# Performance work log

Measured on AMD Instinct MI355X. Metric: run time of the kernel, lower is better.

## Reference

```python
import jax, jax.numpy as jnp
import numpy as np

D_MODEL = 1024
NUM_HEADS = 16
D_K = D_MODEL // NUM_HEADS
B, T = 4, 2048


def setup_inputs() -> dict:
    key = jax.random.key(0)
    ks = jax.random.split(key, 10)
    s = 1.0 / np.sqrt(D_MODEL)
    return {
        "x": jax.random.normal(ks[0], (B, T, D_MODEL), dtype=jnp.float32),
        "attn_mask": jax.random.randint(ks[1], (B, T), 0, 2, dtype=jnp.int32),
        "wq": jax.random.uniform(ks[2], (D_MODEL, D_MODEL), jnp.float32, -s, s),
        "bq": jax.random.uniform(ks[3], (D_MODEL,), jnp.float32, -s, s),
        "wk": jax.random.uniform(ks[4], (D_MODEL, D_MODEL), jnp.float32, -s, s),
        "bk": jax.random.uniform(ks[5], (D_MODEL,), jnp.float32, -s, s),
        "wv": jax.random.uniform(ks[6], (D_MODEL, D_MODEL), jnp.float32, -s, s),
        "bv": jax.random.uniform(ks[7], (D_MODEL,), jnp.float32, -s, s),
        "wo": jax.random.uniform(ks[8], (D_MODEL, D_MODEL), jnp.float32, -s, s),
        "bo": jax.random.uniform(ks[9], (D_MODEL,), jnp.float32, -s, s),
    }


def reference(x, attn_mask, wq, bq, wk, bk, wv, bv, wo, bo):
    b, t, d = x.shape
    h, dk = NUM_HEADS, D_K
    # project and split heads: [B, H, T, Dk]
    q = (x @ wq + bq).reshape(b, t, h, dk).transpose(0, 2, 1, 3)
    k = (x @ wk + bk).reshape(b, t, h, dk).transpose(0, 2, 1, 3)
    v = (x @ wv + bv).reshape(b, t, h, dk).transpose(0, 2, 1, 3)
    scores = jnp.einsum("bhqd,bhkd->bhqk", q, k) / jnp.sqrt(jnp.float32(dk))
    mask = attn_mask[:, None, None, :]  # [B,1,1,T]
    scores = jnp.where(mask == 0, jnp.float32(-1e9), scores)
    attn = jax.nn.softmax(scores, axis=-1)
    out = jnp.einsum("bhqk,bhkd->bhqd", attn, v)
    out = out.transpose(0, 2, 1, 3).reshape(b, t, d)
    return out @ wo + bo
```

## Files before the change

kernel.cpp:

```cpp
#include <hip/hip_runtime.h>
#include <math.h>

#define TT 2048
#define DD 1024
#define HH 16
#define DKK 64
#define BB 4
#define NN 8192

typedef __bf16 bf16x8 __attribute__((ext_vector_type(8)));
typedef float f32x4 __attribute__((ext_vector_type(4)));
typedef float f32x16 __attribute__((ext_vector_type(16)));
typedef unsigned int uint2v __attribute__((ext_vector_type(2)));

#define QSCALE 0.18033688011112043f

__device__ __forceinline__ unsigned short f2bf(float f) {
  unsigned int u = __builtin_bit_cast(unsigned int, f);
  u += 0x7fffu + ((u >> 16) & 1u);
  return (unsigned short)(u >> 16);
}

__device__ __forceinline__ unsigned int cvtpk(float lo, float hi) {
  unsigned int r;
  asm("v_cvt_pk_bf16_f32 %0, %1, %2" : "=v"(r) : "v"(lo), "v"(hi));
  return r;
}

__device__ __forceinline__ void gl_lds16(const void* g, void* s) {
  __builtin_amdgcn_global_load_lds(
      (const __attribute__((address_space(1))) void*)g,
      (__attribute__((address_space(3))) void*)s, 16, 0, 0);
}

#define SWZ(r, byte) ((byte) ^ (((r) & 7) << 4))

__global__ __launch_bounds__(256) void cast_f32_bf16(
    const float* __restrict__ in, unsigned short* __restrict__ out, int n4) {
  int i = blockIdx.x * blockDim.x + threadIdx.x;
  if (i < n4) {
    float4 v = reinterpret_cast<const float4*>(in)[i];
    ushort4 o;
    o.x = f2bf(v.x); o.y = f2bf(v.y); o.z = f2bf(v.z); o.w = f2bf(v.w);
    reinterpret_cast<ushort4*>(out)[i] = o;
  }
}

__global__ __launch_bounds__(256) void wtrans(
    const float* __restrict__ W0, const float* __restrict__ W1,
    const float* __restrict__ W2, const float* __restrict__ W3,
    unsigned short* __restrict__ WT) {
  __shared__ float t[32][33];
  const float* W = (blockIdx.z == 0) ? W0
                   : (blockIdx.z == 1) ? W1
                   : (blockIdx.z == 2) ? W2 : W3;
  unsigned short* O = WT + (size_t)blockIdx.z * DD * DD;
  const int tx = threadIdx.x & 31, ty = threadIdx.x >> 5;
  const int r0 = blockIdx.y * 32, c0 = blockIdx.x * 32;
#pragma unroll
  for (int j = 0; j < 4; ++j)
    t[ty + 8 * j][tx] = W[(size_t)(r0 + ty + 8 * j) * DD + c0 + tx];
  __syncthreads();
#pragma unroll
  for (int j = 0; j < 4; ++j)
    O[(size_t)(c0 + ty + 8 * j) * DD + r0 + tx] = f2bf(t[tx][ty + 8 * j]);
}

__global__ __launch_bounds__(256) void mask_scan(
    const int* __restrict__ mask, int* __restrict__ cm, int* __restrict__ cnt) {
  __shared__ int part[256];
  const int b = blockIdx.x;
  const int tid = threadIdx.x;
  const int* mp = mask + b * TT;
  int loc[8], s = 0;
#pragma unroll
  for (int j = 0; j < 8; ++j) {
    loc[j] = mp[tid * 8 + j] ? 1 : 0;
    s += loc[j];
  }
  part[tid] = s;
  __syncthreads();
  for (int off = 1; off < 256; off <<= 1) {
    const int u = (tid >= off) ? part[tid - off] : 0;
    __syncthreads();
    part[tid] += u;
    __syncthreads();
  }
  if (tid == 255) cnt[b] = part[255];
  int run = part[tid] - s;
#pragma unroll
  for (int j = 0; j < 8; ++j) {
    cm[b * TT + tid * 8 + j] = loc[j] ? (run + 1) : 0;
    run += loc[j];
  }
}

template <int EPI>
__global__ __launch_bounds__(256) void gemm_m97(
    const unsigned short* __restrict__ A, const unsigned short* __restrict__ Bw,
    const float* __restrict__ b0, const float* __restrict__ b1,
    const float* __restrict__ b2, const int* __restrict__ cm,
    unsigned short* __restrict__ O0, unsigned short* __restrict__ O1,
    unsigned short* __restrict__ O2, float* __restrict__ Of) {
  __shared__ unsigned short As[128 * 32];
  __shared__ unsigned short Bs[128 * 32];
  const int tid = threadIdx.x;
  const int l = tid & 63, w = tid >> 6;
  const int ln = l & 15, kg = l >> 4;
  const int wr = w >> 1, wc = w & 1;
  const int rb = blockIdx.x * 128, cb = blockIdx.y * 128;

  f32x4 acc[4][4];
#pragma unroll
  for (int i = 0; i < 4; ++i)
#pragma unroll
    for (int j = 0; j < 4; ++j)
#pragma unroll
      for (int r = 0; r < 4; ++r) acc[i][j][r] = 0.f;

  const int srow = w * 16 + (l >> 2);
  const int sch = (l & 3) * 16;
  const char* Ag = (const char*)A + (size_t)(rb + srow) * 2048 + sch;
  const char* Bg = (const char*)Bw + (size_t)(cb + srow) * 2048 + sch;
  char* Ad = (char*)As + w * 1024;
  char* Bd = (char*)Bs + w * 1024;

  for (int k0 = 0; k0 < 2048; k0 += 64) {
    __syncthreads();
    gl_lds16(Ag + k0, Ad);
    gl_lds16(Ag + k0 + (size_t)64 * 2048, Ad + 4096);
    gl_lds16(Bg + k0, Bd);
    gl_lds16(Bg + k0 + (size_t)64 * 2048, Bd + 4096);
    __syncthreads();
    bf16x8 af[4], bfv[4];
#pragma unroll
    for (int mi = 0; mi < 4; ++mi)
      af[mi] = *reinterpret_cast<const bf16x8*>(
          (const char*)As + (wr * 64 + mi * 16 + ln) * 64 + kg * 16);
#pragma unroll
    for (int ni = 0; ni < 4; ++ni)
      bfv[ni] = *reinterpret_cast<const bf16x8*>(
          (const char*)Bs + (wc * 64 + ni * 16 + ln) * 64 + kg * 16);
#pragma unroll
    for (int mi = 0; mi < 4; ++mi)
#pragma unroll
      for (int ni = 0; ni < 4; ++ni)
        acc[mi][ni] = __builtin_amdgcn_mfma_f32_16x16x32_bf16(
            af[mi], bfv[ni], acc[mi][ni], 0, 0, 0);
  }

  if constexpr (EPI == 0) {
    const int sel = blockIdx.y >> 3;
    const float* bias = sel == 0 ? b0 : (sel == 1 ? b1 : b2);
    const float scale = sel == 0 ? QSCALE : 1.0f;
#pragma unroll
    for (int ni = 0; ni < 4; ++ni) {
      const int c3 = cb + wc * 64 + ni * 16 + ln;
      const int c = c3 & 1023, h = (c3 >> 6) & 15, dk = c3 & 63;
      const float bsv = bias[c];
#pragma unroll
      for (int mi = 0; mi < 4; ++mi) {
#pragma unroll
        for (int r = 0; r < 4; ++r) {
          const int rl = rb + wr * 64 + mi * 16 + kg * 4 + r;
          const int b_ = rl >> 11, t = rl & 2047, bh = b_ * HH + h;
          const unsigned short v = f2bf((acc[mi][ni][r] + bsv) * scale);
          if (sel == 0) {
            O0[(size_t)(bh * 16 + (t >> 7)) * 8192 + (dk >> 3) * 1024 +
               (t & 127) * 8 + (dk & 7)] = v;
          } else {
            const int cmv = cm[b_ * TT + t];
            if (cmv > 0) {
              const int ct = cmv - 1;
              if (sel == 1) {
                O1[(size_t)(bh * 32 + (ct >> 6)) * 4096 + (dk >> 3) * 512 +
                   ((ct >> 5) & 1) * 256 + (ct & 31) * 8 + (dk & 7)] = v;
              } else {
                O2[(size_t)(bh * 32 + (ct >> 6)) * 4096 + ((ct >> 3) & 7) * 512 +
                   (dk >> 5) * 256 + (dk & 31) * 8 + (ct & 7)] = v;
              }
            }
          }
        }
      }
    }
  } else {
#pragma unroll
    for (int ni = 0; ni < 4; ++ni) {
      const int cl = cb + wc * 64 + ni * 16 + ln;
      const float bsv = b0[cl];
#pragma unroll
      for (int mi = 0; mi < 4; ++mi)
#pragma unroll
        for (int r = 0; r < 4; ++r) {
          const int rl = rb + wr * 64 + mi * 16 + kg * 4 + r;
          Of[(size_t)rl * DD + cl] = acc[mi][ni][r] + bsv;
        }
    }
  }
}

template <bool TAIL>
__device__ __forceinline__ void attn_tile10(
    int kt, int n, const char* __restrict__ KU, const char* __restrict__ VU,
    int foff, int hi, const bf16x8 (&qf)[4], f32x16& oc0, f32x16& oc1,
    float& l_) {
  const int ktoff = kt << 13;

  f32x16 sc0, sc1;
#pragma unroll
  for (int i = 0; i < 16; ++i) { sc0[i] = 0.f; sc1[i] = 0.f; }
  __builtin_amdgcn_s_setprio(1);
#pragma unroll
  for (int s = 0; s < 4; ++s) {
    const bf16x8 kf0 =
        *reinterpret_cast<const bf16x8*>(KU + ktoff + foff + s * 2048);
    const bf16x8 kf1 =
        *reinterpret_cast<const bf16x8*>(KU + ktoff + foff + s * 2048 + 512);
    sc0 = __builtin_amdgcn_mfma_f32_32x32x16_bf16(kf0, qf[s], sc0, 0, 0, 0);
    sc1 = __builtin_amdgcn_mfma_f32_32x32x16_bf16(kf1, qf[s], sc1, 0, 0, 0);
  }
  __builtin_amdgcn_s_setprio(0);

  bf16x8 vf[8];
#pragma unroll
  for (int s = 0; s < 4; ++s) {
    vf[2 * s] = *reinterpret_cast<const bf16x8*>(VU + ktoff + foff + s * 2048);
    vf[2 * s + 1] =
        *reinterpret_cast<const bf16x8*>(VU + ktoff + foff + s * 2048 + 512);
  }

#pragma unroll
  for (int i = 0; i < 16; ++i) sc0[i] = __builtin_exp2f(sc0[i]);
#pragma unroll
  for (int i = 0; i < 16; ++i) sc1[i] = __builtin_exp2f(sc1[i]);

  if (TAIL) {
    const int kvb = (kt << 6) + 4 * hi;
#pragma unroll
    for (int i = 0; i < 16; ++i) {
      const int kv0 = kvb + (i & 3) + 8 * (i >> 2);
      sc0[i] = (kv0 < n) ? sc0[i] : 0.f;
      sc1[i] = (kv0 + 32 < n) ? sc1[i] : 0.f;
    }
  }

  {
    const float ra = ((sc0[0] + sc0[1]) + (sc0[2] + sc0[3])) +
                     ((sc0[4] + sc0[5]) + (sc0[6] + sc0[7]));
    const float rb2 = ((sc0[8] + sc0[9]) + (sc0[10] + sc0[11])) +
                      ((sc0[12] + sc0[13]) + (sc0[14] + sc0[15]));
    const float rc = ((sc1[0] + sc1[1]) + (sc1[2] + sc1[3])) +
                     ((sc1[4] + sc1[5]) + (sc1[6] + sc1[7]));
    const float rd = ((sc1[8] + sc1[9]) + (sc1[10] + sc1[11])) +
                     ((sc1[12] + sc1[13]) + (sc1[14] + sc1[15]));
    l_ += (ra + rb2) + (rc + rd);
  }

  bf16x8 pf[4];
#pragma unroll
  for (int s = 0; s < 4; ++s) {
    const int u = s & 1;
    float p0, p1, p2, p3, p4, p5, p6, p7;
    if ((s >> 1) == 0) {
      p0 = sc0[8 * u + 0]; p1 = sc0[8 * u + 1]; p2 = sc0[8 * u + 2];
      p3 = sc0[8 * u + 3]; p4 = sc0[8 * u + 4]; p5 = sc0[8 * u + 5];
      p6 = sc0[8 * u + 6]; p7 = sc0[8 * u + 7];
    } else {
      p0 = sc1[8 * u + 0]; p1 = sc1[8 * u + 1]; p2 = sc1[8 * u + 2];
      p3 = sc1[8 * u + 3]; p4 = sc1[8 * u + 4]; p5 = sc1[8 * u + 5];
      p6 = sc1[8 * u + 6]; p7 = sc1[8 * u + 7];
    }
    const unsigned int wa0 = cvtpk(p0, p1), wa1 = cvtpk(p2, p3);
    const unsigned int wb0 = cvtpk(p4, p5), wb1 = cvtpk(p6, p7);
    const uint2v r0 = __builtin_amdgcn_permlane32_swap(wa0, wb0, false, false);
    const uint2v r1 = __builtin_amdgcn_permlane32_swap(wa1, wb1, false, false);
    union { unsigned int u4[4]; bf16x8 v; } pw;
    pw.u4[0] = r0.x;
    pw.u4[1] = r1.x;
    pw.u4[2] = r0.y;
    pw.u4[3] = r1.y;
    pf[s] = pw.v;
  }

  __builtin_amdgcn_s_setprio(1);
#pragma unroll
  for (int s = 0; s < 4; ++s) {
    oc0 = __builtin_amdgcn_mfma_f32_32x32x16_bf16(vf[2 * s], pf[s], oc0, 0, 0, 0);
    oc1 = __builtin_amdgcn_mfma_f32_32x32x16_bf16(vf[2 * s + 1], pf[s], oc1, 0, 0, 0);
  }
  __builtin_amdgcn_s_setprio(0);
}

__global__ __launch_bounds__(256) void attn_v10(
    const unsigned short* __restrict__ Qt, const unsigned short* __restrict__ Kt,
    const unsigned short* __restrict__ Vt, const int* __restrict__ cnt,
    unsigned short* __restrict__ Ab) {
  const int id = blockIdx.x + 16 * blockIdx.y;
  const int bh = id & 63, qt = id >> 6;
  const int b = bh >> 4, h = bh & 15;

  __shared__ __align__(16) char lds[16384];

  const int tid = threadIdx.x;
  const int l = tid & 63, w = tid >> 6;
  const int ln = l & 31, hi = l >> 5;

  const char* Qtile = (const char*)Qt + (size_t)(bh * 16 + qt) * 16384;
  const char* KU = (const char*)Kt + ((size_t)bh << 18);
  const char* VU = (const char*)Vt + ((size_t)bh << 18);
  const int n = cnt[b];
  const int ntile = (n + 63) >> 6;

  const int qrow = w * 32 + ln;
  bf16x8 qf[4];
#pragma unroll
  for (int s = 0; s < 4; ++s)
    qf[s] = *reinterpret_cast<const bf16x8*>(
        Qtile + (size_t)(s * 2 + hi) * 2048 + qrow * 16);

  const int foff = hi * 1024 + ln * 16;

  f32x16 oc0, oc1;
#pragma unroll
  for (int i = 0; i < 16; ++i) { oc0[i] = 0.f; oc1[i] = 0.f; }
  float l_ = 0.f;

  for (int kt = 0; kt + 1 < ntile; ++kt)
    attn_tile10<false>(kt, n, KU, VU, foff, hi, qf, oc0, oc1, l_);
  attn_tile10<true>(ntile - 1, n, KU, VU, foff, hi, qf, oc0, oc1, l_);

  float ls = l_ + __shfl_xor(l_, 32);
  const float inv = 1.0f / ls;
#pragma unroll
  for (int i = 0; i < 16; ++i) { oc0[i] *= inv; oc1[i] *= inv; }
#pragma unroll
  for (int g = 0; g < 4; ++g) {
    const int d0a = 8 * g + 4 * hi;
    uint2 wv;
    wv.x = cvtpk(oc0[4 * g + 0], oc0[4 * g + 1]);
    wv.y = cvtpk(oc0[4 * g + 2], oc0[4 * g + 3]);
    *reinterpret_cast<uint2*>(lds + qrow * 128 + SWZ(qrow, d0a * 2)) = wv;
    uint2 wv1;
    wv1.x = cvtpk(oc1[4 * g + 0], oc1[4 * g + 1]);
    wv1.y = cvtpk(oc1[4 * g + 2], oc1[4 * g + 3]);
    *reinterpret_cast<uint2*>(lds + qrow * 128 + SWZ(qrow, 64 + d0a * 2)) = wv1;
  }
  __syncthreads();
  {
    const int row2 = tid >> 1, halfc = tid & 1;
    char* gout = (char*)Ab + ((size_t)(b * TT + qt * 128 + row2)) * 2048 +
                 h * 128 + halfc * 64;
#pragma unroll
    for (int u2 = 0; u2 < 4; ++u2) {
      const uint4 d4 = *reinterpret_cast<const uint4*>(
          lds + row2 * 128 + SWZ(row2, halfc * 64 + u2 * 16));
      *reinterpret_cast<uint4*>(gout + u2 * 16) = d4;
    }
  }
}

extern "C" void kernel_launch(void* const* d_in, const int* in_sizes, int n_in,
                              void* d_out, int out_size, void* d_ws,
                              size_t ws_size, hipStream_t stream) {
  const float* x = (const float*)d_in[0];
  const int* attn_mask = (const int*)d_in[1];
  const float* wq = (const float*)d_in[2];
  const float* bq = (const float*)d_in[3];
  const float* wk = (const float*)d_in[4];
  const float* bk = (const float*)d_in[5];
  const float* wv = (const float*)d_in[6];
  const float* bv = (const float*)d_in[7];
  const float* wo = (const float*)d_in[8];
  const float* bo = (const float*)d_in[9];
  float* out = (float*)d_out;

  unsigned short* Xb = (unsigned short*)d_ws;
  unsigned short* WT = Xb + (size_t)NN * DD;
  unsigned short* Qt = WT + (size_t)4 * DD * DD;
  unsigned short* Kt = Qt + (size_t)NN * DD;
  unsigned short* Vt = Kt + (size_t)NN * DD;
  unsigned short* Ab = Vt + (size_t)NN * DD;
  int* cm = (int*)(Ab + (size_t)NN * DD);
  int* cnt = cm + (size_t)BB * TT;

  cast_f32_bf16<<<(NN * DD / 4 + 255) / 256, 256, 0, stream>>>(
      x, Xb, NN * DD / 4);
  wtrans<<<dim3(DD / 32, DD / 32, 4), 256, 0, stream>>>(wq, wk, wv, wo, WT);
  mask_scan<<<BB, 256, 0, stream>>>(attn_mask, cm, cnt);

  gemm_m97<0><<<dim3(NN / 128, 24), 256, 0, stream>>>(
      Xb, WT, bq, bk, bv, cm, Qt, Kt, Vt, nullptr);
  attn_v10<<<dim3(TT / 128, BB * HH), 256, 0, stream>>>(Qt, Kt, Vt, cnt, Ab);
  gemm_m97<1><<<dim3(NN / 128, 8), 256, 0, stream>>>(
      Ab, WT + (size_t)3 * DD * DD, bo, nullptr, nullptr, nullptr, nullptr,
      nullptr, nullptr, out);
}
```

Measured before the change: 192.3 us.

## Gather unmasked rows for K/V projection and deepen GEMM K-tile with swizzled LDS

The mask scan now writes a compacted list of unmasked row indices (rix) instead of a per-row compacted position. The K and V projection blocks gather only unmasked X rows through that list and exit early once past the per-batch count, so roughly half of the K/V GEMM work is skipped. The GEMM also loads 128-wide K slices into a larger, XOR-swizzled LDS tile, which halves the number of sync rounds and is meant to reduce bank conflicts. Risks: tail rows beyond the count in a partial tile read zeroed indices, which point at row 0, and write padded slots, which relies on the attention kernel masking by n. The attention kernel now guards the n==0 case.

```diff
diff --git a/kernel.cpp b/kernel.cpp
--- a/kernel.cpp
+++ b/kernel.cpp
@@ -67,11 +67,12 @@
 }
 
 __global__ __launch_bounds__(256) void mask_scan(
-    const int* __restrict__ mask, int* __restrict__ cm, int* __restrict__ cnt) {
+    const int* __restrict__ mask, int* __restrict__ rix, int* __restrict__ cnt) {
   __shared__ int part[256];
   const int b = blockIdx.x;
   const int tid = threadIdx.x;
   const int* mp = mask + b * TT;
+  for (int i = tid; i < TT; i += 256) rix[b * TT + i] = 0;
   int loc[8], s = 0;
 #pragma unroll
   for (int j = 0; j < 8; ++j) {
@@ -90,25 +91,51 @@
   int run = part[tid] - s;
 #pragma unroll
   for (int j = 0; j < 8; ++j) {
-    cm[b * TT + tid * 8 + j] = loc[j] ? (run + 1) : 0;
+    if (loc[j]) rix[b * TT + run] = tid * 8 + j;
     run += loc[j];
   }
 }
 
 template <int EPI>
-__global__ __launch_bounds__(256) void gemm_m97(
+__global__ __launch_bounds__(256) void gemm_v11(
     const unsigned short* __restrict__ A, const unsigned short* __restrict__ Bw,
     const float* __restrict__ b0, const float* __restrict__ b1,
-    const float* __restrict__ b2, const int* __restrict__ cm,
-    unsigned short* __restrict__ O0, unsigned short* __restrict__ O1,
-    unsigned short* __restrict__ O2, float* __restrict__ Of) {
-  __shared__ unsigned short As[128 * 32];
-  __shared__ unsigned short Bs[128 * 32];
+    const float* __restrict__ b2, const int* __restrict__ rix,
+    const int* __restrict__ cnt, unsigned short* __restrict__ O0,
+    unsigned short* __restrict__ O1, unsigned short* __restrict__ O2,
+    float* __restrict__ Of) {
+  __shared__ unsigned short As[128 * 64];
+  __shared__ unsigned short Bs[128 * 64];
   const int tid = threadIdx.x;
   const int l = tid & 63, w = tid >> 6;
   const int ln = l & 15, kg = l >> 4;
   const int wr = w >> 1, wc = w & 1;
   const int rb = blockIdx.x * 128, cb = blockIdx.y * 128;
+  const int sel = (EPI == 0) ? (blockIdx.y >> 3) : 0;
+  const int b_ = rb >> 11;
+
+  const int sr = w * 8 + (l >> 3);
+  const int sch = ((l & 7) * 16) ^ (((l >> 3) & 7) << 4);
+
+  const char* Ag[4];
+  if (EPI == 0 && sel > 0) {
+    const int rbl = rb & 2047;
+    if (rbl >= cnt[b_]) return;
+    const int* rixb = rix + (b_ << 11);
+#pragma unroll
+    for (int j = 0; j < 4; ++j) {
+      const int r = rixb[rbl + j * 32 + sr];
+      Ag[j] = (const char*)A + ((size_t)((b_ << 11) + r) * 2048) + sch;
+    }
+  } else {
+#pragma unroll
+    for (int j = 0; j < 4; ++j)
+      Ag[j] = (const char*)A + ((size_t)(rb + j * 32 + sr) * 2048) + sch;
+  }
+  const char* Bg[4];
+#pragma unroll
+  for (int j = 0; j < 4; ++j)
+    Bg[j] = (const char*)Bw + ((size_t)(cb + j * 32 + sr) * 2048) + sch;
 
   f32x4 acc[4][4];
 #pragma unroll
@@ -118,39 +145,39 @@
 #pragma unroll
       for (int r = 0; r < 4; ++r) acc[i][j][r] = 0.f;
 
-  const int srow = w * 16 + (l >> 2);
-  const int sch = (l & 3) * 16;
-  const char* Ag = (const char*)A + (size_t)(rb + srow) * 2048 + sch;
-  const char* Bg = (const char*)Bw + (size_t)(cb + srow) * 2048 + sch;
-  char* Ad = (char*)As + w * 1024;
-  char* Bd = (char*)Bs + w * 1024;
-
-  for (int k0 = 0; k0 < 2048; k0 += 64) {
+  for (int kb = 0; kb < 2048; kb += 128) {
     __syncthreads();
-    gl_lds16(Ag + k0, Ad);
-    gl_lds16(Ag + k0 + (size_t)64 * 2048, Ad + 4096);
-    gl_lds16(Bg + k0, Bd);
-    gl_lds16(Bg + k0 + (size_t)64 * 2048, Bd + 4096);
+#pragma unroll
+    for (int j = 0; j < 4; ++j) {
+      gl_lds16(Ag[j] + kb, (char*)As + j * 4096 + w * 1024);
+      gl_lds16(Bg[j] + kb, (char*)Bs + j * 4096 + w * 1024);
+    }
     __syncthreads();
-    bf16x8 af[4], bfv[4];
-#pragma unroll
-    for (int mi = 0; mi < 4; ++mi)
-      af[mi] = *reinterpret_cast<const bf16x8*>(
-          (const char*)As + (wr * 64 + mi * 16 + ln) * 64 + kg * 16);
-#pragma unroll
-    for (int ni = 0; ni < 4; ++ni)
-      bfv[ni] = *reinterpret_cast<const bf16x8*>(
-          (const char*)Bs + (wc * 64 + ni * 16 + ln) * 64 + kg * 16);
-#pragma unroll
-    for (int mi = 0; mi < 4; ++mi)
-#pragma unroll
-      for (int ni = 0; ni < 4; ++ni)
-        acc[mi][ni] = __builtin_amdgcn_mfma_f32_16x16x32_bf16(
-            af[mi], bfv[ni], acc[mi][ni], 0, 0, 0);
+#pragma unroll
+    for (int ks = 0; ks < 2; ++ks) {
+      bf16x8 af[4], bfv[4];
+#pragma unroll
+      for (int mi = 0; mi < 4; ++mi) {
+        const int row = wr * 64 + mi * 16 + ln;
+        af[mi] = *reinterpret_cast<const bf16x8*>(
+            (const char*)As + row * 128 + SWZ(row, ks * 64 + kg * 16));
+      }
+#pragma unroll
+      for (int ni = 0; ni < 4; ++ni) {
+        const int row = wc * 64 + ni * 16 + ln;
+        bfv[ni] = *reinterpret_cast<const bf16x8*>(
+            (const char*)Bs + row * 128 + SWZ(row, ks * 64 + kg * 16));
+      }
+#pragma unroll
+      for (int mi = 0; mi < 4; ++mi)
+#pragma unroll
+        for (int ni = 0; ni < 4; ++ni)
+          acc[mi][ni] = __builtin_amdgcn_mfma_f32_16x16x32_bf16(
+              af[mi], bfv[ni], acc[mi][ni], 0, 0, 0);
+    }
   }
 
   if constexpr (EPI == 0) {
-    const int sel = blockIdx.y >> 3;
     const float* bias = sel == 0 ? b0 : (sel == 1 ? b1 : b2);
     const float scale = sel == 0 ? QSCALE : 1.0f;
 #pragma unroll
@@ -158,28 +185,22 @@
       const int c3 = cb + wc * 64 + ni * 16 + ln;
       const int c = c3 & 1023, h = (c3 >> 6) & 15, dk = c3 & 63;
       const float bsv = bias[c];
+      const int bh = b_ * HH + h;
 #pragma unroll
       for (int mi = 0; mi < 4; ++mi) {
 #pragma unroll
         for (int r = 0; r < 4; ++r) {
-          const int rl = rb + wr * 64 + mi * 16 + kg * 4 + r;
-          const int b_ = rl >> 11, t = rl & 2047, bh = b_ * HH + h;
+          const int rl = (rb & 2047) + wr * 64 + mi * 16 + kg * 4 + r;
           const unsigned short v = f2bf((acc[mi][ni][r] + bsv) * scale);
           if (sel == 0) {
-            O0[(size_t)(bh * 16 + (t >> 7)) * 8192 + (dk >> 3) * 1024 +
-               (t & 127) * 8 + (dk & 7)] = v;
+            O0[(size_t)(bh * 16 + (rl >> 7)) * 8192 + (dk >> 3) * 1024 +
+               (rl & 127) * 8 + (dk & 7)] = v;
+          } else if (sel == 1) {
+            O1[(size_t)(bh * 32 + (rl >> 6)) * 4096 + (dk >> 3) * 512 +
+               ((rl >> 5) & 1) * 256 + (rl & 31) * 8 + (dk & 7)] = v;
           } else {
-            const int cmv = cm[b_ * TT + t];
-            if (cmv > 0) {
-              const int ct = cmv - 1;
-              if (sel == 1) {
-                O1[(size_t)(bh * 32 + (ct >> 6)) * 4096 + (dk >> 3) * 512 +
-                   ((ct >> 5) & 1) * 256 + (ct & 31) * 8 + (dk & 7)] = v;
-              } else {
-                O2[(size_t)(bh * 32 + (ct >> 6)) * 4096 + ((ct >> 3) & 7) * 512 +
-                   (dk >> 5) * 256 + (dk & 31) * 8 + (ct & 7)] = v;
-              }
-            }
+            O2[(size_t)(bh * 32 + (rl >> 6)) * 4096 + ((rl >> 3) & 7) * 512 +
+               (dk >> 5) * 256 + (dk & 31) * 8 + (rl & 7)] = v;
           }
         }
       }
@@ -310,7 +331,7 @@
   const char* KU = (const char*)Kt + ((size_t)bh << 18);
   const char* VU = (const char*)Vt + ((size_t)bh << 18);
   const int n = cnt[b];
-  const int ntile = (n + 63) >> 6;
+  const int ntile = (n > 0) ? ((n + 63) >> 6) : 1;
 
   const int qrow = w * 32 + ln;
   bf16x8 qf[4];
@@ -381,18 +402,18 @@
   unsigned short* Kt = Qt + (size_t)NN * DD;
   unsigned short* Vt = Kt + (size_t)NN * DD;
   unsigned short* Ab = Vt + (size_t)NN * DD;
-  int* cm = (int*)(Ab + (size_t)NN * DD);
-  int* cnt = cm + (size_t)BB * TT;
+  int* rix = (int*)(Ab + (size_t)NN * DD);
+  int* cnt = rix + (size_t)BB * TT;
 
   cast_f32_bf16<<<(NN * DD / 4 + 255) / 256, 256, 0, stream>>>(
       x, Xb, NN * DD / 4);
   wtrans<<<dim3(DD / 32, DD / 32, 4), 256, 0, stream>>>(wq, wk, wv, wo, WT);
-  mask_scan<<<BB, 256, 0, stream>>>(attn_mask, cm, cnt);
-
-  gemm_m97<0><<<dim3(NN / 128, 24), 256, 0, stream>>>(
-      Xb, WT, bq, bk, bv, cm, Qt, Kt, Vt, nullptr);
+  mask_scan<<<BB, 256, 0, stream>>>(attn_mask, rix, cnt);
+
+  gemm_v11<0><<<dim3(NN / 128, 24), 256, 0, stream>>>(
+      Xb, WT, bq, bk, bv, rix, cnt, Qt, Kt, Vt, nullptr);
   attn_v10<<<dim3(TT / 128, BB * HH), 256, 0, stream>>>(Qt, Kt, Vt, cnt, Ab);
-  gemm_m97<1><<<dim3(NN / 128, 8), 256, 0, stream>>>(
+  gemm_v11<1><<<dim3(NN / 128, 8), 256, 0, stream>>>(
       Ab, WT + (size_t)3 * DD * DD, bo, nullptr, nullptr, nullptr, nullptr,
-      nullptr, nullptr, out);
-}
+      nullptr, nullptr, nullptr, out);
+}
```

After: 171.7 us, median of 5. 10.7% less time.

## Gather unmasked rows into K/V projection GEMM and skip masked row blocks

Applied to the files above, without the earlier changes.

The mask scan now writes a compacted list of unmasked token indices instead of a per-token rank map. The K and V projection blocks gather only those rows through per-thread source pointers and exit early when the block lies beyond the unmasked count, which removes the projection work spent on masked keys. The attention kernel is guarded against a zero count, and the GEMM template is split into separate QKV and output kernels. Partial tail blocks read zero-padded index entries, so they compute on row 0 and write values into padding slots.

```diff
diff --git a/kernel.cpp b/kernel.cpp
--- a/kernel.cpp
+++ b/kernel.cpp
@@ -67,11 +67,12 @@
 }
 
 __global__ __launch_bounds__(256) void mask_scan(
-    const int* __restrict__ mask, int* __restrict__ cm, int* __restrict__ cnt) {
+    const int* __restrict__ mask, int* __restrict__ rix, int* __restrict__ cnt) {
   __shared__ int part[256];
   const int b = blockIdx.x;
   const int tid = threadIdx.x;
   const int* mp = mask + b * TT;
+  for (int i = tid; i < TT; i += 256) rix[b * TT + i] = 0;
   int loc[8], s = 0;
 #pragma unroll
   for (int j = 0; j < 8; ++j) {
@@ -90,18 +91,17 @@
   int run = part[tid] - s;
 #pragma unroll
   for (int j = 0; j < 8; ++j) {
-    cm[b * TT + tid * 8 + j] = loc[j] ? (run + 1) : 0;
+    if (loc[j]) rix[b * TT + run] = tid * 8 + j;
     run += loc[j];
   }
 }
 
-template <int EPI>
-__global__ __launch_bounds__(256) void gemm_m97(
+__global__ __launch_bounds__(256) void gemm_qkv32(
     const unsigned short* __restrict__ A, const unsigned short* __restrict__ Bw,
     const float* __restrict__ b0, const float* __restrict__ b1,
-    const float* __restrict__ b2, const int* __restrict__ cm,
-    unsigned short* __restrict__ O0, unsigned short* __restrict__ O1,
-    unsigned short* __restrict__ O2, float* __restrict__ Of) {
+    const float* __restrict__ b2, const int* __restrict__ rix,
+    const int* __restrict__ cnt, unsigned short* __restrict__ O0,
+    unsigned short* __restrict__ O1, unsigned short* __restrict__ O2) {
   __shared__ unsigned short As[128 * 32];
   __shared__ unsigned short Bs[128 * 32];
   const int tid = threadIdx.x;
@@ -109,6 +109,33 @@
   const int ln = l & 15, kg = l >> 4;
   const int wr = w >> 1, wc = w & 1;
   const int rb = blockIdx.x * 128, cb = blockIdx.y * 128;
+  const int sel = blockIdx.y >> 3;
+  const int b_ = rb >> 11, rbl = rb & 2047;
+
+  const int srow = w * 16 + (l >> 2);
+  const int sch = (l & 3) * 16;
+
+  const char* Ag[2];
+  if (sel > 0) {
+    if (rbl >= cnt[b_]) return;
+    const int* rixb = rix + (b_ << 11);
+#pragma unroll
+    for (int j = 0; j < 2; ++j) {
+      const int r = rixb[rbl + j * 64 + srow];
+      Ag[j] = (const char*)A + ((size_t)((b_ << 11) + r) * 2048) + sch;
+    }
+  } else {
+#pragma unroll
+    for (int j = 0; j < 2; ++j)
+      Ag[j] = (const char*)A + ((size_t)(rb + j * 64 + srow) * 2048) + sch;
+  }
+  const char* Bg[2];
+#pragma unroll
+  for (int j = 0; j < 2; ++j)
+    Bg[j] = (const char*)Bw + ((size_t)(cb + j * 64 + srow) * 2048) + sch;
+
+  char* Ad = (char*)As + w * 1024;
+  char* Bd = (char*)Bs + w * 1024;
 
   f32x4 acc[4][4];
 #pragma unroll
@@ -117,6 +144,71 @@
     for (int j = 0; j < 4; ++j)
 #pragma unroll
       for (int r = 0; r < 4; ++r) acc[i][j][r] = 0.f;
+
+  for (int k0 = 0; k0 < 2048; k0 += 64) {
+    __syncthreads();
+    gl_lds16(Ag[0] + k0, Ad);
+    gl_lds16(Ag[1] + k0, Ad + 4096);
+    gl_lds16(Bg[0] + k0, Bd);
+    gl_lds16(Bg[1] + k0, Bd + 4096);
+    __syncthreads();
+    bf16x8 af[4], bfv[4];
+#pragma unroll
+    for (int mi = 0; mi < 4; ++mi)
+      af[mi] = *reinterpret_cast<const bf16x8*>(
+          (const char*)As + (wr * 64 + mi * 16 + ln) * 64 + kg * 16);
+#pragma unroll
+    for (int ni = 0; ni < 4; ++ni)
+      bfv[ni] = *reinterpret_cast<const bf16x8*>(
+          (const char*)Bs + (wc * 64 + ni * 16 + ln) * 64 + kg * 16);
+#pragma unroll
+    for (int mi = 0; mi < 4; ++mi)
+#pragma unroll
+      for (int ni = 0; ni < 4; ++ni)
+        acc[mi][ni] = __builtin_amdgcn_mfma_f32_16x16x32_bf16(
+            af[mi], bfv[ni], acc[mi][ni], 0, 0, 0);
+  }
+
+  const float* bias = sel == 0 ? b0 : (sel == 1 ? b1 : b2);
+  const float scale = sel == 0 ? QSCALE : 1.0f;
+  const int bhb = b_ * HH;
+#pragma unroll
+  for (int ni = 0; ni < 4; ++ni) {
+    const int c3 = cb + wc * 64 + ni * 16 + ln;
+    const int c = c3 & 1023, h = (c3 >> 6) & 15, dk = c3 & 63;
+    const float bsv = bias[c];
+    const int bh = bhb + h;
+#pragma unroll
+    for (int mi = 0; mi < 4; ++mi) {
+#pragma unroll
+      for (int r = 0; r < 4; ++r) {
+        const int rl = rbl + wr * 64 + mi * 16 + kg * 4 + r;
+        const unsigned short v = f2bf((acc[mi][ni][r] + bsv) * scale);
+        if (sel == 0) {
+          O0[(size_t)(bh * 16 + (rl >> 7)) * 8192 + (dk >> 3) * 1024 +
+             (rl & 127) * 8 + (dk & 7)] = v;
+        } else if (sel == 1) {
+          O1[(size_t)(bh * 32 + (rl >> 6)) * 4096 + (dk >> 3) * 512 +
+             ((rl >> 5) & 1) * 256 + (rl & 31) * 8 + (dk & 7)] = v;
+        } else {
+          O2[(size_t)(bh * 32 + (rl >> 6)) * 4096 + ((rl >> 3) & 7) * 512 +
+             (dk >> 5) * 256 + (dk & 31) * 8 + (rl & 7)] = v;
+        }
+      }
+    }
+  }
+}
+
+__global__ __launch_bounds__(256) void gemm_out32(
+    const unsigned short* __restrict__ A, const unsigned short* __restrict__ Bw,
+    const float* __restrict__ bias, float* __restrict__ Of) {
+  __shared__ unsigned short As[128 * 32];
+  __shared__ unsigned short Bs[128 * 32];
+  const int tid = threadIdx.x;
+  const int l = tid & 63, w = tid >> 6;
+  const int ln = l & 15, kg = l >> 4;
+  const int wr = w >> 1, wc = w & 1;
+  const int rb = blockIdx.x * 128, cb = blockIdx.y * 128;
 
   const int srow = w * 16 + (l >> 2);
   const int sch = (l & 3) * 16;
@@ -125,6 +217,14 @@
   char* Ad = (char*)As + w * 1024;
   char* Bd = (char*)Bs + w * 1024;
 
+  f32x4 acc[4][4];
+#pragma unroll
+  for (int i = 0; i < 4; ++i)
+#pragma unroll
+    for (int j = 0; j < 4; ++j)
+#pragma unroll
+      for (int r = 0; r < 4; ++r) acc[i][j][r] = 0.f;
+
   for (int k0 = 0; k0 < 2048; k0 += 64) {
     __syncthreads();
     gl_lds16(Ag + k0, Ad);
@@ -149,54 +249,17 @@
             af[mi], bfv[ni], acc[mi][ni], 0, 0, 0);
   }
 
-  if constexpr (EPI == 0) {
-    const int sel = blockIdx.y >> 3;
-    const float* bias = sel == 0 ? b0 : (sel == 1 ? b1 : b2);
-    const float scale = sel == 0 ? QSCALE : 1.0f;
-#pragma unroll
-    for (int ni = 0; ni < 4; ++ni) {
-      const int c3 = cb + wc * 64 + ni * 16 + ln;
-      const int c = c3 & 1023, h = (c3 >> 6) & 15, dk = c3 & 63;
-      const float bsv = bias[c];
-#pragma unroll
-      for (int mi = 0; mi < 4; ++mi) {
-#pragma unroll
-        for (int r = 0; r < 4; ++r) {
-          const int rl = rb + wr * 64 + mi * 16 + kg * 4 + r;
-          const int b_ = rl >> 11, t = rl & 2047, bh = b_ * HH + h;
-          const unsigned short v = f2bf((acc[mi][ni][r] + bsv) * scale);
-          if (sel == 0) {
-            O0[(size_t)(bh * 16 + (t >> 7)) * 8192 + (dk >> 3) * 1024 +
-               (t & 127) * 8 + (dk & 7)] = v;
-          } else {
-            const int cmv = cm[b_ * TT + t];
-            if (cmv > 0) {
-              const int ct = cmv - 1;
-              if (sel == 1) {
-                O1[(size_t)(bh * 32 + (ct >> 6)) * 4096 + (dk >> 3) * 512 +
-                   ((ct >> 5) & 1) * 256 + (ct & 31) * 8 + (dk & 7)] = v;
-              } else {
-                O2[(size_t)(bh * 32 + (ct >> 6)) * 4096 + ((ct >> 3) & 7) * 512 +
-                   (dk >> 5) * 256 + (dk & 31) * 8 + (ct & 7)] = v;
-              }
-            }
-          }
-        }
+#pragma unroll
+  for (int ni = 0; ni < 4; ++ni) {
+    const int cl = cb + wc * 64 + ni * 16 + ln;
+    const float bsv = bias[cl];
+#pragma unroll
+    for (int mi = 0; mi < 4; ++mi)
+#pragma unroll
+      for (int r = 0; r < 4; ++r) {
+        const int rl = rb + wr * 64 + mi * 16 + kg * 4 + r;
+        Of[(size_t)rl * DD + cl] = acc[mi][ni][r] + bsv;
       }
-    }
-  } else {
-#pragma unroll
-    for (int ni = 0; ni < 4; ++ni) {
-      const int cl = cb + wc * 64 + ni * 16 + ln;
-      const float bsv = b0[cl];
-#pragma unroll
-      for (int mi = 0; mi < 4; ++mi)
-#pragma unroll
-        for (int r = 0; r < 4; ++r) {
-          const int rl = rb + wr * 64 + mi * 16 + kg * 4 + r;
-          Of[(size_t)rl * DD + cl] = acc[mi][ni][r] + bsv;
-        }
-    }
   }
 }
 
@@ -310,7 +373,7 @@
   const char* KU = (const char*)Kt + ((size_t)bh << 18);
   const char* VU = (const char*)Vt + ((size_t)bh << 18);
   const int n = cnt[b];
-  const int ntile = (n + 63) >> 6;
+  const int ntile = (n > 0) ? ((n + 63) >> 6) : 1;
 
   const int qrow = w * 32 + ln;
   bf16x8 qf[4];
@@ -381,18 +444,17 @@
   unsigned short* Kt = Qt + (size_t)NN * DD;
   unsigned short* Vt = Kt + (size_t)NN * DD;
   unsigned short* Ab = Vt + (size_t)NN * DD;
-  int* cm = (int*)(Ab + (size_t)NN * DD);
-  int* cnt = cm + (size_t)BB * TT;
+  int* rix = (int*)(Ab + (size_t)NN * DD);
+  int* cnt = rix + (size_t)BB * TT;
 
   cast_f32_bf16<<<(NN * DD / 4 + 255) / 256, 256, 0, stream>>>(
       x, Xb, NN * DD / 4);
   wtrans<<<dim3(DD / 32, DD / 32, 4), 256, 0, stream>>>(wq, wk, wv, wo, WT);
-  mask_scan<<<BB, 256, 0, stream>>>(attn_mask, cm, cnt);
-
-  gemm_m97<0><<<dim3(NN / 128, 24), 256, 0, stream>>>(
-      Xb, WT, bq, bk, bv, cm, Qt, Kt, Vt, nullptr);
+  mask_scan<<<BB, 256, 0, stream>>>(attn_mask, rix, cnt);
+
+  gemm_qkv32<<<dim3(NN / 128, 24), 256, 0, stream>>>(
+      Xb, WT, bq, bk, bv, rix, cnt, Qt, Kt, Vt);
   attn_v10<<<dim3(TT / 128, BB * HH), 256, 0, stream>>>(Qt, Kt, Vt, cnt, Ab);
-  gemm_m97<1><<<dim3(NN / 128, 8), 256, 0, stream>>>(
-      Ab, WT + (size_t)3 * DD * DD, bo, nullptr, nullptr, nullptr, nullptr,
-      nullptr, nullptr, out);
-}
+  gemm_out32<<<dim3(NN / 128, 8), 256, 0, stream>>>(
+      Ab, WT + (size_t)3 * DD * DD, bo, out);
+}
```

Measured after the change: 186.9 us. 1.03x faster.
